# Performance work log

Measured on AMD Instinct MI355X. Metric: run time of the kernel, lower is better.

The kernel has to match this reference:

```python
import jax, jax.numpy as jnp
import numpy as np
import math

M_MICRO = 8    # n_micro
CELLS = 1024   # cells per micro engine (n_cells // n_micro)
DIM = 512      # hidden_dim (complex state dim)
IN_DIM = 512   # input_dim == hidden_dim so torch's F.interpolate branch is skipped


def _build_neighbors(n):
    """Hypercube bit-flip + ring topology, deduped, padded to max degree."""
    n_bits = max(1, int(math.ceil(math.log2(n))))
    lists = []
    for i in range(n):
        s = set()
        for b in range(n_bits):
            j = i ^ (1 << b)
            if 0 <= j < n:
                s.add(j)
        s.add((i + 1) % n)
        s.add((i - 1) % n)
        lists.append(sorted(s))
    K = max(len(l) for l in lists)
    idx = np.zeros((n, K), dtype=np.int32)
    mask = np.zeros((n, K), dtype=np.float32)
    for i, l in enumerate(lists):
        idx[i, : len(l)] = l
        mask[i, : len(l)] = 1.0
    return idx, mask


def _forward(x, step, amp0, phase0, phase_vel, nbr_idx, nbr_mask, macro_h0,
             w_ih, b_ih, w_hh, b_hh, wq, bq, wk, bk, wv, bv, out_w, out_b):
    sig = x.reshape(-1)                    # [DIM]; input_dim == dim -> no interpolation
    t = step * 0.1
    states0 = amp0 * jnp.exp(1j * phase0)  # complex64 [M, n, d]

    def micro_step(st, pv):
        # phase-velocity rotation
        st = st * jnp.exp(1j * (pv * 0.1))
        ang = jnp.angle(st)
        nb_s = st[nbr_idx]                 # [n, K, d] neighbor gather
        nb_a = ang[nbr_idx]
        coupling = jnp.cos(ang[:, None, :] - nb_a)
        interf = jnp.sum(coupling * nb_s * nbr_mask[:, :, None], axis=1) * 0.1
        cnt = jnp.maximum(nbr_mask.sum(axis=1), 1.0)
        new = 0.7 * st + 0.3 * interf / cnt[:, None]
        # category morphism from strongest neighbor (selected on pre-interference states)
        absum = jnp.abs(st).sum(axis=-1)
        score = jnp.where(nbr_mask > 0, absum[nbr_idx], -jnp.inf)
        sel = jnp.argmax(score, axis=1)
        midx = jnp.take_along_axis(nbr_idx, sel[:, None], axis=1)[:, 0]
        src = st[midx]
        morph = jnp.abs(src) * jnp.exp(1j * (jnp.angle(new) - jnp.angle(src)))
        new = new + 0.02 * morph
        # global wave modulation
        i_arr = jnp.arange(new.shape[0], dtype=jnp.float32)
        wave = 0.02 * jnp.sin(t + 2.0 * math.pi * i_arr / new.shape[0])
        new = new * (1.0 + wave)[:, None]
        # signal phase perturbation (per-cell decaying scale)
        sig_norm = sig / (jnp.abs(sig).max() + 1e-8)
        pp = sig_norm * (math.pi * 0.1)
        scale = 0.1 / (1.0 + 0.1 * i_arr)
        newang = jnp.angle(new) + pp[None, :] * scale[:, None]
        # amplitude renormalization
        amp = jnp.abs(new)
        amp = amp / (amp.max(axis=-1, keepdims=True) + 1e-8)
        return amp * jnp.exp(1j * newang)

    states = jax.vmap(micro_step)(states0, phase_vel)  # [M, n, d]
    # micro outputs and coherences are .detach()'ed / .item()'ed in torch
    micro_out = jax.lax.stop_gradient(jnp.abs(states).mean(axis=1))          # [M, d]
    coh = jax.lax.stop_gradient(
        jnp.abs(jnp.exp(1j * jnp.angle(states)).mean(axis=1)).mean(axis=1))  # [M]
    # GRUCell (torch gate order: r, z, n)
    gx = micro_out @ w_ih.T + b_ih
    gh = macro_h0 @ w_hh.T + b_hh
    rx, zx, nx = jnp.split(gx, 3, axis=1)
    rh, zh, nh = jnp.split(gh, 3, axis=1)
    r = jax.nn.sigmoid(rx + rh)
    z = jax.nn.sigmoid(zx + zh)
    ng = jnp.tanh(nx + r * nh)
    h = jax.lax.stop_gradient((1.0 - z) * ng + z * macro_h0)  # detached macro hiddens
    H = h.shape[1]
    Q = h @ wq.T + bq
    K = h @ wk.T + bk
    V = h @ wv.T + bv
    scores = (Q @ K.T) / math.sqrt(H)
    scores = scores * (0.5 + 0.5 * coh[None, :] * coh[:, None])
    attn = jax.nn.softmax(scores, axis=-1)
    attended = (attn @ V).mean(axis=0, keepdims=True)  # [1, H]
    # faction sync/debate (updates hidden state; feeds only tension here)
    n_f = 4
    fs = h.shape[0] // n_f
    hh = h.reshape(n_f, fs, -1)
    hh = 0.85 * hh + 0.15 * hh.mean(axis=1, keepdims=True)
    if step > 5:
        go = hh.mean(axis=1).mean(axis=0)
        dc = max(1, fs // 4)
        hh = hh.at[:, :dc].set(0.85 * hh[:, :dc] + 0.15 * go)
    h2 = hh.reshape(h.shape)
    pred = attended @ out_w.T + out_b  # [1, IN_DIM]
    tension = jnp.var(h2, ddof=1)      # torch .var() is unbiased
    return pred, tension


def setup_inputs():
    key = jax.random.key(0)
    k = jax.random.split(key, 20)
    M, n, d, H, IN = M_MICRO, CELLS, DIM, DIM, IN_DIM
    amp0 = jax.random.uniform(k[0], (M, n, d)) * 0.5 + 0.5
    base = jnp.linspace(0.0, 2.0 * math.pi, d)
    gidx = jnp.arange(M * n, dtype=jnp.float32).reshape(M, n)
    off = 2.0 * math.pi * gidx / (n * 8)
    phase0 = base[None, None, :] + off[..., None] + jax.random.normal(k[1], (M, n, d)) * 0.3
    phase_vel = jax.random.normal(k[2], (M, n, d)) * 0.05
    nbr_idx, nbr_mask = _build_neighbors(n)
    macro_h0 = jax.random.normal(k[3], (M, H)) * 0.1
    s = 1.0 / math.sqrt(H)
    u = lambda kk, shape: jax.random.uniform(kk, shape, minval=-s, maxval=s)
    return {
        "x": jax.random.normal(k[4], (1, IN)),
        "step": 0,
        "amp0": amp0, "phase0": phase0, "phase_vel": phase_vel,
        "nbr_idx": jnp.asarray(nbr_idx), "nbr_mask": jnp.asarray(nbr_mask),
        "macro_h0": macro_h0,
        "w_ih": u(k[5], (3 * H, H)), "b_ih": u(k[6], (3 * H,)),
        "w_hh": u(k[7], (3 * H, H)), "b_hh": u(k[8], (3 * H,)),
        "wq": u(k[9], (H, H)), "bq": u(k[10], (H,)),
        "wk": u(k[11], (H, H)), "bk": u(k[12], (H,)),
        "wv": u(k[13], (H, H)), "bv": u(k[14], (H,)),
        "out_w": u(k[15], (IN, H)), "out_b": u(k[16], (IN,)),
    }


def reference(x, step, amp0, phase0, phase_vel, nbr_idx, nbr_mask, macro_h0,
              w_ih, b_ih, w_hh, b_hh, wq, bq, wk, bk, wv, bv, out_w, out_b):
    return _forward(x, step, amp0, phase0, phase_vel, nbr_idx, nbr_mask, macro_h0,
                    w_ih, b_ih, w_hh, b_hh, wq, bq, wk, bk, wv, bv, out_w, out_b)
```

## Files before the change

kernel.cpp:

```cpp
#include <hip/hip_runtime.h>
#include <hip/hip_fp16.h>
#include <math.h>

#define M_  8
#define N_  1024
#define D_  512
#define H_  512
#define PI_ 3.14159265358979323846f

static const size_t OFF_CHS = 0;
static const size_t OFF_SIG = OFF_CHS + (size_t)M_*N_*D_;
static const size_t OFF_MA  = OFF_SIG + 64;
static const size_t OFF_MZR = OFF_MA  + (size_t)M_*D_;
static const size_t OFF_MZI = OFF_MZR + (size_t)M_*D_;
static const size_t OFF_H   = OFF_MZI + (size_t)M_*D_;
static const size_t OFF_Q   = OFF_H   + (size_t)M_*H_;
static const size_t OFF_K   = OFF_Q   + (size_t)M_*H_;
static const size_t OFF_V   = OFF_K   + (size_t)M_*H_;
static const size_t OFF_ATT = OFF_V   + (size_t)M_*H_;
static const size_t FAST_FLOATS = OFF_ATT + 512;
static const size_t FB_SIG = 0;
static const size_t FB_MA  = FB_SIG + 64;
static const size_t FB_MZR = FB_MA  + (size_t)M_*D_;
static const size_t FB_MZI = FB_MZR + (size_t)M_*D_;
static const size_t FB_H   = FB_MZI + (size_t)M_*D_;
static const size_t FB_Q   = FB_H   + (size_t)M_*H_;
static const size_t FB_K   = FB_Q   + (size_t)M_*H_;
static const size_t FB_V   = FB_K   + (size_t)M_*H_;
static const size_t FB_ATT = FB_V   + (size_t)M_*H_;

struct F8   { float4 a, b; };
struct H2x8 { __half2 h[8]; };

__device__ __forceinline__ void unp8(float* d, const F8& v) {
    d[0]=v.a.x; d[1]=v.a.y; d[2]=v.a.z; d[3]=v.a.w;
    d[4]=v.b.x; d[5]=v.b.y; d[6]=v.b.z; d[7]=v.b.w;
}


__global__ __launch_bounds__(256) void prep_kernel(const float* __restrict__ phase0,
                                                   const float* __restrict__ pv,
                                                   const float* __restrict__ x,
                                                   __half2* __restrict__ chs,
                                                   float* __restrict__ acczero,
                                                   float* __restrict__ sigmax) {
    const int bid = blockIdx.x, tid = threadIdx.x;
    if (bid < 2048) {
        const size_t e = ((size_t)bid * 256 + tid) * 8;
        float ph[8], pw[8];
        unp8(ph, *reinterpret_cast<const F8*>(phase0 + e));
        unp8(pw, *reinterpret_cast<const F8*>(pv + e));
        H2x8 out;
        #pragma unroll
        for (int s = 0; s < 8; ++s) {
            const float th = fmaf(0.1f, pw[s], ph[s]);
            out.h[s] = __floats2half2_rn(__cosf(th), __sinf(th));
        }
        *reinterpret_cast<H2x8*>(chs + e) = out;
        if (bid < 6) {
            F8 z; z.a = make_float4(0.f,0.f,0.f,0.f); z.b = z.a;
            *reinterpret_cast<F8*>(acczero + (size_t)bid * 2048 + (size_t)tid * 8) = z;
        }
    } else if (tid < 64) {
        float v[8];
        unp8(v, *reinterpret_cast<const F8*>(x + (size_t)tid * 8));
        float mx = 0.f;
        #pragma unroll
        for (int s = 0; s < 8; ++s) mx = fmaxf(mx, fabsf(v[s]));
        #pragma unroll
        for (int off = 32; off; off >>= 1) mx = fmaxf(mx, __shfl_down(mx, off));
        if (tid == 0) *sigmax = mx;
    }
}

__global__ __launch_bounds__(512) void micro_kernel(
    const float* __restrict__ amp0, const __half2* __restrict__ chs,
    const float* __restrict__ x, const float* __restrict__ sigmax_p,
    const int* __restrict__ nbr_idx, const float* __restrict__ nbr_mask,
    const int* __restrict__ step_p,
    float* __restrict__ mA, float* __restrict__ mZr, float* __restrict__ mZi, int K)
{
    const int m = blockIdx.x & 7;
    const int g = blockIdx.x >> 3;
    const int wid  = threadIdx.x >> 6;
    const int lane = threadIdx.x & 63;
    const int i = (g << 3) + wid;

    __shared__ float accA[D_], accZr[D_], accZi[D_];
    for (int idx = threadIdx.x; idx < D_; idx += 512) { accA[idx]=0.f; accZr[idx]=0.f; accZi[idx]=0.f; }
    __syncthreads();

    const float t  = 0.1f * (float)(*step_p);
    const float sm = *sigmax_p;

    float pp[8];
    unp8(pp, *reinterpret_cast<const F8*>(x + (size_t)lane * 8));
    #pragma unroll
    for (int s = 0; s < 8; ++s) pp[s] = pp[s] / (sm + 1e-8f) * (PI_ * 0.1f);

    const size_t mrow = (size_t)m * N_;

    int L = 0;
    for (int k = 0; k < K; ++k) L += (nbr_mask[i * K + k] > 0.f) ? 1 : 0;

    float SA[8], SB[8], SC[8];
    #pragma unroll
    for (int s = 0; s < 8; ++s) { SA[s]=0.f; SB[s]=0.f; SC[s]=0.f; }
    float best = -1e30f; int midx = 0;

    for (int k = 0; k < L; ++k) {
        const int nb = nbr_idx[i * K + k];
        const size_t noff = (mrow + nb) * (size_t)D_ + (size_t)lane * 8;
        float aN[8];
        unp8(aN, *reinterpret_cast<const F8*>(amp0 + noff));
        const H2x8 hx = *reinterpret_cast<const H2x8*>(chs + noff);
        #pragma unroll
        for (int s = 0; s < 8; ++s) {
            const float2 cs = __half22float2(hx.h[s]);
            const float ac = aN[s] * cs.x, as_ = aN[s] * cs.y;
            SA[s] = fmaf(ac,  cs.x, SA[s]);
            SB[s] = fmaf(ac,  cs.y, SB[s]);
            SC[s] = fmaf(as_, cs.y, SC[s]);
        }
        float rs = ((aN[0]+aN[1])+(aN[2]+aN[3])) + ((aN[4]+aN[5])+(aN[6]+aN[7]));
        #pragma unroll
        for (int off = 1; off < 64; off <<= 1) rs += __shfl_xor(rs, off);
        const bool sel = rs > best;
        best = sel ? rs : best;
        midx = sel ? nb : midx;
    }
    const float f = 0.03f / fmaxf((float)L, 1.f);

    float nre[8], nim[8];
    {
        const size_t ooff = (mrow + i) * (size_t)D_ + (size_t)lane * 8;
        float aO[8];
        unp8(aO, *reinterpret_cast<const F8*>(amp0 + ooff));
        const H2x8 hx = *reinterpret_cast<const H2x8*>(chs + ooff);
        #pragma unroll
        for (int s = 0; s < 8; ++s) {
            const float2 cs = __half22float2(hx.h[s]);
            nre[s] = 0.7f * aO[s] * cs.x + f * (cs.x * SA[s] + cs.y * SB[s]);
            nim[s] = 0.7f * aO[s] * cs.y + f * (cs.x * SB[s] + cs.y * SC[s]);
        }
    }
    {
        const size_t soff = (mrow + midx) * (size_t)D_ + (size_t)lane * 8;
        float aS[8];
        unp8(aS, *reinterpret_cast<const F8*>(amp0 + soff));
        const H2x8 hx = *reinterpret_cast<const H2x8*>(chs + soff);
        #pragma unroll
        for (int s = 0; s < 8; ++s) {
            const float2 cs = __half22float2(hx.h[s]);
            const float sre = aS[s] * cs.x, sim = aS[s] * cs.y;
            const float inv = __builtin_amdgcn_rcpf(sqrtf(nre[s]*nre[s] + nim[s]*nim[s]));
            const float mre = (nre[s] * sre + nim[s] * sim) * inv;
            const float mim = (nim[s] * sre - nre[s] * sim) * inv;
            nre[s] = fmaf(0.02f, mre, nre[s]);
            nim[s] = fmaf(0.02f, mim, nim[s]);
        }
    }

    const float wf = 1.f + 0.02f * __sinf(t + 2.f * PI_ * (float)i / (float)N_);
    const float scale_i = 0.1f / (1.f + 0.1f * (float)i);

    float ampn[8], rm = 0.f;
    #pragma unroll
    for (int s = 0; s < 8; ++s) {
        nre[s] *= wf; nim[s] *= wf;
        ampn[s] = sqrtf(nre[s]*nre[s] + nim[s]*nim[s]);
        rm = fmaxf(rm, ampn[s]);
    }
    #pragma unroll
    for (int off = 1; off < 64; off <<= 1) rm = fmaxf(rm, __shfl_xor(rm, off));
    const float rinv = __builtin_amdgcn_rcpf(rm + 1e-8f);

    #pragma unroll
    for (int s = 0; s < 8; ++s) {
        const float anorm = ampn[s] * rinv;
        const float iamp  = __builtin_amdgcn_rcpf(ampn[s]);
        const float ure = nre[s] * iamp, uim = nim[s] * iamp;
        const float d  = pp[s] * scale_i;
        const float d2 = d * d;
        const float cd = 1.f - 0.5f * d2;
        const float sd = d * (1.f - 0.16666667f * d2);
        const int p = (s << 6) + lane;
        atomicAdd(&accA[p],  anorm);
        atomicAdd(&accZr[p], ure * cd - uim * sd);
        atomicAdd(&accZi[p], ure * sd + uim * cd);
    }
    __syncthreads();
    const int j = threadIdx.x;
    const int p = ((j & 7) << 6) + (j >> 3);
    atomicAdd(&mA [m * D_ + j], accA[p]);
    atomicAdd(&mZr[m * D_ + j], accZr[p]);
    atomicAdd(&mZi[m * D_ + j], accZi[p]);
}


__global__ __launch_bounds__(256) void zero_sig_kernel(const float* __restrict__ x,
                                                       float* __restrict__ acczero,
                                                       float* __restrict__ sigmax) {
    const int bid = blockIdx.x, tid = threadIdx.x;
    if (bid < 6) {
        F8 z; z.a = make_float4(0.f,0.f,0.f,0.f); z.b = z.a;
        *reinterpret_cast<F8*>(acczero + (size_t)bid * 2048 + (size_t)tid * 8) = z;
    } else if (tid < 64) {
        float v[8];
        unp8(v, *reinterpret_cast<const F8*>(x + (size_t)tid * 8));
        float mx = 0.f;
        #pragma unroll
        for (int s = 0; s < 8; ++s) mx = fmaxf(mx, fabsf(v[s]));
        #pragma unroll
        for (int off = 32; off; off >>= 1) mx = fmaxf(mx, __shfl_down(mx, off));
        if (tid == 0) *sigmax = mx;
    }
}

__global__ __launch_bounds__(512) void micro_fb_kernel(
    const float* __restrict__ amp0, const float* __restrict__ phase0,
    const float* __restrict__ pvel,
    const float* __restrict__ x, const float* __restrict__ sigmax_p,
    const int* __restrict__ nbr_idx, const float* __restrict__ nbr_mask,
    const int* __restrict__ step_p,
    float* __restrict__ mA, float* __restrict__ mZr, float* __restrict__ mZi, int K)
{
    const int m = blockIdx.x & 7;
    const int g = blockIdx.x >> 3;
    const int wid  = threadIdx.x >> 6;
    const int lane = threadIdx.x & 63;
    const int i = (g << 3) + wid;

    __shared__ float accA[D_], accZr[D_], accZi[D_];
    for (int idx = threadIdx.x; idx < D_; idx += 512) { accA[idx]=0.f; accZr[idx]=0.f; accZi[idx]=0.f; }
    __syncthreads();

    const float t  = 0.1f * (float)(*step_p);
    const float sm = *sigmax_p;

    float pp[8];
    unp8(pp, *reinterpret_cast<const F8*>(x + (size_t)lane * 8));
    #pragma unroll
    for (int s = 0; s < 8; ++s) pp[s] = pp[s] / (sm + 1e-8f) * (PI_ * 0.1f);

    const size_t mrow = (size_t)m * N_;

    int L = 0;
    for (int k = 0; k < K; ++k) L += (nbr_mask[i * K + k] > 0.f) ? 1 : 0;

    float SA[8], SB[8], SC[8];
    #pragma unroll
    for (int s = 0; s < 8; ++s) { SA[s]=0.f; SB[s]=0.f; SC[s]=0.f; }
    float best = -1e30f; int midx = 0;

    for (int k = 0; k < L; ++k) {
        const int nb = nbr_idx[i * K + k];
        const size_t noff = (mrow + nb) * (size_t)D_ + (size_t)lane * 8;
        float aN[8], phN[8], pwN[8];
        unp8(aN, *reinterpret_cast<const F8*>(amp0 + noff));
        unp8(phN, *reinterpret_cast<const F8*>(phase0 + noff));
        unp8(pwN, *reinterpret_cast<const F8*>(pvel + noff));
        #pragma unroll
        for (int s = 0; s < 8; ++s) {
            const float th = fmaf(0.1f, pwN[s], phN[s]);
            const float cn = __cosf(th), sn = __sinf(th);
            const float ac = aN[s] * cn, as_ = aN[s] * sn;
            SA[s] = fmaf(ac,  cn, SA[s]);
            SB[s] = fmaf(ac,  sn, SB[s]);
            SC[s] = fmaf(as_, sn, SC[s]);
        }
        float rs = ((aN[0]+aN[1])+(aN[2]+aN[3])) + ((aN[4]+aN[5])+(aN[6]+aN[7]));
        #pragma unroll
        for (int off = 1; off < 64; off <<= 1) rs += __shfl_xor(rs, off);
        const bool sel = rs > best;
        best = sel ? rs : best;
        midx = sel ? nb : midx;
    }
    const float f = 0.03f / fmaxf((float)L, 1.f);

    float nre[8], nim[8];
    {
        const size_t ooff = (mrow + i) * (size_t)D_ + (size_t)lane * 8;
        float aO[8], ph[8], pw[8];
        unp8(aO, *reinterpret_cast<const F8*>(amp0 + ooff));
        unp8(ph, *reinterpret_cast<const F8*>(phase0 + ooff));
        unp8(pw, *reinterpret_cast<const F8*>(pvel + ooff));
        #pragma unroll
        for (int s = 0; s < 8; ++s) {
            const float th = fmaf(0.1f, pw[s], ph[s]);
            const float c = __cosf(th), sn = __sinf(th);
            nre[s] = 0.7f * aO[s] * c  + f * (c * SA[s] + sn * SB[s]);
            nim[s] = 0.7f * aO[s] * sn + f * (c * SB[s] + sn * SC[s]);
        }
    }
    {
        const size_t soff = (mrow + midx) * (size_t)D_ + (size_t)lane * 8;
        float aS[8], ph[8], pw[8];
        unp8(aS, *reinterpret_cast<const F8*>(amp0 + soff));
        unp8(ph, *reinterpret_cast<const F8*>(phase0 + soff));
        unp8(pw, *reinterpret_cast<const F8*>(pvel + soff));
        #pragma unroll
        for (int s = 0; s < 8; ++s) {
            const float th = fmaf(0.1f, pw[s], ph[s]);
            const float c = __cosf(th), sn = __sinf(th);
            const float sre = aS[s] * c, sim = aS[s] * sn;
            const float inv = __builtin_amdgcn_rcpf(sqrtf(nre[s]*nre[s] + nim[s]*nim[s]));
            const float mre = (nre[s] * sre + nim[s] * sim) * inv;
            const float mim = (nim[s] * sre - nre[s] * sim) * inv;
            nre[s] = fmaf(0.02f, mre, nre[s]);
            nim[s] = fmaf(0.02f, mim, nim[s]);
        }
    }

    const float wf = 1.f + 0.02f * __sinf(t + 2.f * PI_ * (float)i / (float)N_);
    const float scale_i = 0.1f / (1.f + 0.1f * (float)i);

    float ampn[8], rm = 0.f;
    #pragma unroll
    for (int s = 0; s < 8; ++s) {
        nre[s] *= wf; nim[s] *= wf;
        ampn[s] = sqrtf(nre[s]*nre[s] + nim[s]*nim[s]);
        rm = fmaxf(rm, ampn[s]);
    }
    #pragma unroll
    for (int off = 1; off < 64; off <<= 1) rm = fmaxf(rm, __shfl_xor(rm, off));
    const float rinv = __builtin_amdgcn_rcpf(rm + 1e-8f);

    #pragma unroll
    for (int s = 0; s < 8; ++s) {
        const float anorm = ampn[s] * rinv;
        const float iamp  = __builtin_amdgcn_rcpf(ampn[s]);
        const float ure = nre[s] * iamp, uim = nim[s] * iamp;
        const float d  = pp[s] * scale_i;
        const float d2 = d * d;
        const float cd = 1.f - 0.5f * d2;
        const float sd = d * (1.f - 0.16666667f * d2);
        const int p = (s << 6) + lane;
        atomicAdd(&accA[p],  anorm);
        atomicAdd(&accZr[p], ure * cd - uim * sd);
        atomicAdd(&accZi[p], ure * sd + uim * cd);
    }
    __syncthreads();
    const int j = threadIdx.x;
    const int p = ((j & 7) << 6) + (j >> 3);
    atomicAdd(&mA [m * D_ + j], accA[p]);
    atomicAdd(&mZr[m * D_ + j], accZr[p]);
    atomicAdd(&mZi[m * D_ + j], accZi[p]);
}


__global__ __launch_bounds__(256) void macro_kernel(
    const float* __restrict__ mA, const float* __restrict__ h0,
    const float* __restrict__ w_ih, const float* __restrict__ b_ih,
    const float* __restrict__ w_hh, const float* __restrict__ b_hh,
    float* __restrict__ h)
{
    __shared__ float vx[M_ * H_], vh[M_ * H_];
    for (int idx = threadIdx.x; idx < M_ * H_; idx += 256) {
        vx[idx] = mA[idx] * (1.f / (float)N_);
        vh[idx] = h0[idx];
    }
    __syncthreads();
    const int wid = threadIdx.x >> 6, lane = threadIdx.x & 63;
    const int d = (blockIdx.x << 2) + wid;
    float wr[6][8];
    #pragma unroll
    for (int rr = 0; rr < 3; ++rr) {
        const size_t row = (size_t)(d + rr * H_) * H_;
        #pragma unroll
        for (int kk = 0; kk < 8; ++kk) {
            wr[rr][kk]     = w_ih[row + kk * 64 + lane];
            wr[rr + 3][kk] = w_hh[row + kk * 64 + lane];
        }
    }
    const float br = b_ih[d], bz = b_ih[d + H_], bn = b_ih[d + 2 * H_];
    const float dr = b_hh[d], dz = b_hh[d + H_], dn = b_hh[d + 2 * H_];
    for (int m = 0; m < M_; ++m) {
        float acc[6] = {0.f, 0.f, 0.f, 0.f, 0.f, 0.f};
        #pragma unroll
        for (int kk = 0; kk < 8; ++kk) {
            const float xm = vx[m * H_ + kk * 64 + lane];
            const float hm = vh[m * H_ + kk * 64 + lane];
            acc[0] = fmaf(wr[0][kk], xm, acc[0]);
            acc[1] = fmaf(wr[1][kk], xm, acc[1]);
            acc[2] = fmaf(wr[2][kk], xm, acc[2]);
            acc[3] = fmaf(wr[3][kk], hm, acc[3]);
            acc[4] = fmaf(wr[4][kk], hm, acc[4]);
            acc[5] = fmaf(wr[5][kk], hm, acc[5]);
        }
        #pragma unroll
        for (int off = 32; off; off >>= 1)
            #pragma unroll
            for (int q = 0; q < 6; ++q) acc[q] += __shfl_down(acc[q], off);
        if (lane == 0) {
            const float r  = 1.f / (1.f + expf(-(acc[0] + br + acc[3] + dr)));
            const float z  = 1.f / (1.f + expf(-(acc[1] + bz + acc[4] + dz)));
            const float ng = tanhf(acc[2] + bn + r * (acc[5] + dn));
            h[m * H_ + d] = (1.f - z) * ng + z * vh[m * H_ + d];
        }
    }
}

__global__ void qkv_kernel(const float* __restrict__ h,
                           const float* __restrict__ wq, const float* __restrict__ bq,
                           const float* __restrict__ wk, const float* __restrict__ bk,
                           const float* __restrict__ wv, const float* __restrict__ bv,
                           float* __restrict__ Q, float* __restrict__ Kk, float* __restrict__ V) {
    __shared__ float hv[M_ * H_];
    for (int idx = threadIdx.x; idx < M_ * H_; idx += blockDim.x) hv[idx] = h[idx];
    __syncthreads();
    const int gr = (blockIdx.x << 2) + (threadIdx.x >> 6);
    const int lane = threadIdx.x & 63;
    const int which = gr / H_, r = gr % H_;
    const float* W = (which == 0) ? wq : ((which == 1) ? wk : wv);
    const float* B = (which == 0) ? bq : ((which == 1) ? bk : bv);
    float* O       = (which == 0) ? Q  : ((which == 1) ? Kk : V);
    float wvv[8];
    #pragma unroll
    for (int kk = 0; kk < 8; ++kk) wvv[kk] = W[(size_t)r * H_ + kk * 64 + lane];
    for (int m = 0; m < M_; ++m) {
        float acc = 0.f;
        #pragma unroll
        for (int kk = 0; kk < 8; ++kk) acc = fmaf(wvv[kk], hv[m * H_ + kk * 64 + lane], acc);
        for (int off = 32; off; off >>= 1) acc += __shfl_down(acc, off);
        if (lane == 0) O[m * H_ + r] = acc + B[r];
    }
}

__global__ void attn_faction_kernel(const float* __restrict__ Q, const float* __restrict__ Kk,
                                    const float* __restrict__ V,
                                    const float* __restrict__ mZr, const float* __restrict__ mZi,
                                    const float* __restrict__ h, const int* __restrict__ step_p,
                                    float* __restrict__ attended, float* __restrict__ out_tension) {
    const int tid = threadIdx.x;
    __shared__ float coh_sm[M_];
    {
        const int w = tid >> 6, lane = tid & 63;
        float s = 0.f;
        #pragma unroll
        for (int q = 0; q < 8; ++q) {
            const int j = lane + (q << 6);
            const float zr = mZr[w * D_ + j], zi = mZi[w * D_ + j];
            s += sqrtf(zr * zr + zi * zi);
        }
        #pragma unroll
        for (int off = 32; off; off >>= 1) s += __shfl_down(s, off);
        if (lane == 0) coh_sm[w] = s * (1.f / ((float)N_ * (float)D_));
    }
    __syncthreads();
    {
        const int j = tid;
        const int step = *step_p;
        float h2[M_];
        #pragma unroll
        for (int ff = 0; ff < 4; ++ff) {
            const float a = h[(2*ff) * H_ + j], b = h[(2*ff+1) * H_ + j];
            const float mn = 0.5f * (a + b);
            h2[2*ff]   = 0.85f * a + 0.15f * mn;
            h2[2*ff+1] = 0.85f * b + 0.15f * mn;
        }
        if (step > 5) {
            float go = 0.f;
            #pragma unroll
            for (int m = 0; m < M_; ++m) go += h2[m];
            go *= (1.f / (float)M_);
            #pragma unroll
            for (int ff = 0; ff < 4; ++ff) h2[2*ff] = 0.85f * h2[2*ff] + 0.15f * go;
        }
        float sum = 0.f, sq = 0.f;
        #pragma unroll
        for (int m = 0; m < M_; ++m) { sum += h2[m]; sq = fmaf(h2[m], h2[m], sq); }
        __shared__ float rs[D_], rq[D_];
        rs[j] = sum; rq[j] = sq;
        __syncthreads();
        for (int s = D_/2; s > 0; s >>= 1) {
            if (j < s) { rs[j] += rs[j + s]; rq[j] += rq[j + s]; }
            __syncthreads();
        }
        if (j == 0) {
            const float Nt = (float)(M_ * H_);
            const float mean = rs[0] / Nt;
            out_tension[0] = (rq[0] - Nt * mean * mean) / (Nt - 1.f);
        }
        __syncthreads();
    }
    __shared__ float sc[M_][M_];
    __shared__ float colw[M_];
    const int a = tid >> 6, lane = tid & 63;
    for (int b = 0; b < M_; ++b) {
        float acc = 0.f;
        #pragma unroll
        for (int kk = 0; kk < 8; ++kk) acc = fmaf(Q[a * H_ + kk * 64 + lane], Kk[b * H_ + kk * 64 + lane], acc);
        for (int off = 32; off; off >>= 1) acc += __shfl_down(acc, off);
        if (lane == 0) sc[a][b] = acc * rsqrtf((float)H_) * (0.5f + 0.5f * coh_sm[a] * coh_sm[b]);
    }
    __syncthreads();
    if (tid < M_) {
        float mx = -1e30f;
        for (int b = 0; b < M_; ++b) mx = fmaxf(mx, sc[tid][b]);
        float e[M_], smm = 0.f;
        for (int b = 0; b < M_; ++b) { e[b] = expf(sc[tid][b] - mx); smm += e[b]; }
        for (int b = 0; b < M_; ++b) sc[tid][b] = e[b] / smm;
    }
    __syncthreads();
    if (tid < M_) {
        float sum = 0.f;
        for (int a2 = 0; a2 < M_; ++a2) sum += sc[a2][tid];
        colw[tid] = sum * (1.f / (float)M_);
    }
    __syncthreads();
    float acc = 0.f;
    #pragma unroll
    for (int b = 0; b < M_; ++b) acc = fmaf(colw[b], V[b * H_ + tid], acc);
    attended[tid] = acc;
}

__global__ void pred_kernel(const float* __restrict__ attended,
                            const float* __restrict__ out_w, const float* __restrict__ out_b,
                            float* __restrict__ pred) {
    __shared__ float av[H_];
    for (int idx = threadIdx.x; idx < H_; idx += blockDim.x) av[idx] = attended[idx];
    __syncthreads();
    const int p = (blockIdx.x << 2) + (threadIdx.x >> 6);
    const int lane = threadIdx.x & 63;
    float acc = 0.f;
    #pragma unroll
    for (int kk = 0; kk < 8; ++kk) acc = fmaf(av[kk * 64 + lane], out_w[(size_t)p * H_ + kk * 64 + lane], acc);
    for (int off = 32; off; off >>= 1) acc += __shfl_down(acc, off);
    if (lane == 0) pred[p] = acc + out_b[p];
}


extern "C" void kernel_launch(void* const* d_in, const int* in_sizes, int n_in,
                              void* d_out, int out_size, void* d_ws, size_t ws_size,
                              hipStream_t stream) {
    const float* x      = (const float*)d_in[0];
    const int*   step   = (const int*)  d_in[1];
    const float* amp0   = (const float*)d_in[2];
    const float* phase0 = (const float*)d_in[3];
    const float* pvel   = (const float*)d_in[4];
    const int*   nbr_i  = (const int*)  d_in[5];
    const float* nbr_m  = (const float*)d_in[6];
    const float* h0     = (const float*)d_in[7];
    const float* w_ih   = (const float*)d_in[8];
    const float* b_ih   = (const float*)d_in[9];
    const float* w_hh   = (const float*)d_in[10];
    const float* b_hh   = (const float*)d_in[11];
    const float* wq     = (const float*)d_in[12];
    const float* bq     = (const float*)d_in[13];
    const float* wk     = (const float*)d_in[14];
    const float* bk     = (const float*)d_in[15];
    const float* wv     = (const float*)d_in[16];
    const float* bv     = (const float*)d_in[17];
    const float* out_w  = (const float*)d_in[18];
    const float* out_b  = (const float*)d_in[19];
    float* out = (float*)d_out;

    const int K = in_sizes[5] / N_;
    float* ws = (float*)d_ws;

    if (ws_size >= FAST_FLOATS * sizeof(float)) {
        __half2* wCHS = (__half2*)(ws + OFF_CHS);
        float* wSIG = ws + OFF_SIG;
        float* wMA  = ws + OFF_MA;
        float* wMZR = ws + OFF_MZR;
        float* wMZI = ws + OFF_MZI;
        float* wH   = ws + OFF_H;
        float* wQ   = ws + OFF_Q;
        float* wK   = ws + OFF_K;
        float* wV   = ws + OFF_V;
        float* wATT = ws + OFF_ATT;

        prep_kernel<<<2049, 256, 0, stream>>>(phase0, pvel, x, wCHS, wMA, wSIG);
        micro_kernel<<<1024, 512, 0, stream>>>(amp0, wCHS, x, wSIG, nbr_i, nbr_m, step,
                                               wMA, wMZR, wMZI, K);
        macro_kernel<<<128, 256, 0, stream>>>(wMA, h0, w_ih, b_ih, w_hh, b_hh, wH);
        qkv_kernel<<<384, 256, 0, stream>>>(wH, wq, bq, wk, bk, wv, bv, wQ, wK, wV);
        attn_faction_kernel<<<1, 512, 0, stream>>>(wQ, wK, wV, wMZR, wMZI, wH, step, wATT, out + 512);
        pred_kernel<<<128, 256, 0, stream>>>(wATT, out_w, out_b, out);
    } else {
        float* wSIG = ws + FB_SIG;
        float* wMA  = ws + FB_MA;
        float* wMZR = ws + FB_MZR;
        float* wMZI = ws + FB_MZI;
        float* wH   = ws + FB_H;
        float* wQ   = ws + FB_Q;
        float* wK   = ws + FB_K;
        float* wV   = ws + FB_V;
        float* wATT = ws + FB_ATT;

        zero_sig_kernel<<<7, 256, 0, stream>>>(x, wMA, wSIG);
        micro_fb_kernel<<<1024, 512, 0, stream>>>(amp0, phase0, pvel, x, wSIG, nbr_i, nbr_m, step,
                                                  wMA, wMZR, wMZI, K);
        macro_kernel<<<128, 256, 0, stream>>>(wMA, h0, w_ih, b_ih, w_hh, b_hh, wH);
        qkv_kernel<<<384, 256, 0, stream>>>(wH, wq, bq, wk, bk, wv, bv, wQ, wK, wV);
        attn_faction_kernel<<<1, 512, 0, stream>>>(wQ, wK, wV, wMZR, wMZI, wH, step, wATT, out + 512);
        pred_kernel<<<128, 256, 0, stream>>>(wATT, out_w, out_b, out);
    }
}
```

Measured before the change: 252.4 us.

## Precompute per-cell amplitude sums in prep and process two cells per wave

The prep kernel now also reads amp0 and writes a per-cell amplitude sum into a new workspace region. The micro kernel uses those sums to pick the strongest neighbor instead of doing a 64-lane shuffle reduction for every neighbor. Each wave now handles two cells, with blocks shrunk to 256 threads. Per-cell contributions are summed in registers before the shared-memory atomics, halving those atomics. In exchange, prep reads amp0 once more, register pressure roughly doubles with two sets of accumulators, and there are fewer waves in flight.

```diff
diff --git a/kernel.cpp b/kernel.cpp
--- a/kernel.cpp
+++ b/kernel.cpp
@@ -13,7 +13,8 @@
 static const size_t OFF_MA  = OFF_SIG + 64;
 static const size_t OFF_MZR = OFF_MA  + (size_t)M_*D_;
 static const size_t OFF_MZI = OFF_MZR + (size_t)M_*D_;
-static const size_t OFF_H   = OFF_MZI + (size_t)M_*D_;
+static const size_t OFF_ABS = OFF_MZI + (size_t)M_*D_;
+static const size_t OFF_H   = OFF_ABS + (size_t)M_*N_;
 static const size_t OFF_Q   = OFF_H   + (size_t)M_*H_;
 static const size_t OFF_K   = OFF_Q   + (size_t)M_*H_;
 static const size_t OFF_V   = OFF_K   + (size_t)M_*H_;
@@ -38,18 +39,21 @@
 }
 
 
-__global__ __launch_bounds__(256) void prep_kernel(const float* __restrict__ phase0,
+__global__ __launch_bounds__(256) void prep_kernel(const float* __restrict__ amp0,
+                                                   const float* __restrict__ phase0,
                                                    const float* __restrict__ pv,
                                                    const float* __restrict__ x,
                                                    __half2* __restrict__ chs,
                                                    float* __restrict__ acczero,
+                                                   float* __restrict__ absum,
                                                    float* __restrict__ sigmax) {
     const int bid = blockIdx.x, tid = threadIdx.x;
     if (bid < 2048) {
         const size_t e = ((size_t)bid * 256 + tid) * 8;
-        float ph[8], pw[8];
+        float ph[8], pw[8], av[8];
         unp8(ph, *reinterpret_cast<const F8*>(phase0 + e));
         unp8(pw, *reinterpret_cast<const F8*>(pv + e));
+        unp8(av, *reinterpret_cast<const F8*>(amp0 + e));
         H2x8 out;
         #pragma unroll
         for (int s = 0; s < 8; ++s) {
@@ -57,6 +61,10 @@
             out.h[s] = __floats2half2_rn(__cosf(th), __sinf(th));
         }
         *reinterpret_cast<H2x8*>(chs + e) = out;
+        float rs = ((av[0]+av[1])+(av[2]+av[3])) + ((av[4]+av[5])+(av[6]+av[7]));
+        #pragma unroll
+        for (int off = 32; off; off >>= 1) rs += __shfl_down(rs, off);
+        if ((tid & 63) == 0) absum[bid * 4 + (tid >> 6)] = rs;
         if (bid < 6) {
             F8 z; z.a = make_float4(0.f,0.f,0.f,0.f); z.b = z.a;
             *reinterpret_cast<F8*>(acczero + (size_t)bid * 2048 + (size_t)tid * 8) = z;
@@ -73,21 +81,26 @@
     }
 }
 
-__global__ __launch_bounds__(512) void micro_kernel(
+__global__ __launch_bounds__(256) void micro_kernel(
     const float* __restrict__ amp0, const __half2* __restrict__ chs,
     const float* __restrict__ x, const float* __restrict__ sigmax_p,
     const int* __restrict__ nbr_idx, const float* __restrict__ nbr_mask,
-    const int* __restrict__ step_p,
+    const int* __restrict__ step_p, const float* __restrict__ absum,
     float* __restrict__ mA, float* __restrict__ mZr, float* __restrict__ mZi, int K)
 {
     const int m = blockIdx.x & 7;
     const int g = blockIdx.x >> 3;
     const int wid  = threadIdx.x >> 6;
     const int lane = threadIdx.x & 63;
-    const int i = (g << 3) + wid;
+    const int i0 = (g << 3) + (wid << 1);
+    const int i1 = i0 + 1;
 
     __shared__ float accA[D_], accZr[D_], accZi[D_];
-    for (int idx = threadIdx.x; idx < D_; idx += 512) { accA[idx]=0.f; accZr[idx]=0.f; accZi[idx]=0.f; }
+    {
+        const int j = threadIdx.x;
+        accA[j] = 0.f; accZr[j] = 0.f; accZi[j] = 0.f;
+        accA[j+256] = 0.f; accZr[j+256] = 0.f; accZi[j+256] = 0.f;
+    }
     __syncthreads();
 
     const float t  = 0.1f * (float)(*step_p);
@@ -99,102 +112,144 @@
     for (int s = 0; s < 8; ++s) pp[s] = pp[s] / (sm + 1e-8f) * (PI_ * 0.1f);
 
     const size_t mrow = (size_t)m * N_;
-
-    int L = 0;
-    for (int k = 0; k < K; ++k) L += (nbr_mask[i * K + k] > 0.f) ? 1 : 0;
-
-    float SA[8], SB[8], SC[8];
-    #pragma unroll
-    for (int s = 0; s < 8; ++s) { SA[s]=0.f; SB[s]=0.f; SC[s]=0.f; }
-    float best = -1e30f; int midx = 0;
-
-    for (int k = 0; k < L; ++k) {
-        const int nb = nbr_idx[i * K + k];
-        const size_t noff = (mrow + nb) * (size_t)D_ + (size_t)lane * 8;
-        float aN[8];
-        unp8(aN, *reinterpret_cast<const F8*>(amp0 + noff));
-        const H2x8 hx = *reinterpret_cast<const H2x8*>(chs + noff);
+    const size_t lo = (size_t)lane * 8;
+
+    int L0 = 0, L1 = 0;
+    for (int k = 0; k < K; ++k) {
+        L0 += (nbr_mask[i0 * K + k] > 0.f) ? 1 : 0;
+        L1 += (nbr_mask[i1 * K + k] > 0.f) ? 1 : 0;
+    }
+    const int Lmax = (L0 > L1) ? L0 : L1;
+
+    float SA0[8], SB0[8], SC0[8], SA1[8], SB1[8], SC1[8];
+    #pragma unroll
+    for (int s = 0; s < 8; ++s) {
+        SA0[s]=0.f; SB0[s]=0.f; SC0[s]=0.f;
+        SA1[s]=0.f; SB1[s]=0.f; SC1[s]=0.f;
+    }
+    float best0 = -1e30f, best1 = -1e30f; int mi0 = 0, mi1 = 0;
+
+    for (int k = 0; k < Lmax; ++k) {
+        const bool v0 = (k < L0), v1 = (k < L1);
+        const int nb0 = v0 ? nbr_idx[i0 * K + k] : 0;
+        const int nb1 = v1 ? nbr_idx[i1 * K + k] : 0;
+        const size_t off0 = (mrow + nb0) * (size_t)D_ + lo;
+        const size_t off1 = (mrow + nb1) * (size_t)D_ + lo;
+        float a0[8], a1[8];
+        unp8(a0, *reinterpret_cast<const F8*>(amp0 + off0));
+        const H2x8 h0 = *reinterpret_cast<const H2x8*>(chs + off0);
+        unp8(a1, *reinterpret_cast<const F8*>(amp0 + off1));
+        const H2x8 h1 = *reinterpret_cast<const H2x8*>(chs + off1);
+        if (v0) {
+            #pragma unroll
+            for (int s = 0; s < 8; ++s) {
+                const float2 cs = __half22float2(h0.h[s]);
+                const float ac = a0[s] * cs.x, as_ = a0[s] * cs.y;
+                SA0[s] = fmaf(ac,  cs.x, SA0[s]);
+                SB0[s] = fmaf(ac,  cs.y, SB0[s]);
+                SC0[s] = fmaf(as_, cs.y, SC0[s]);
+            }
+            const float sc = absum[mrow + nb0];
+            if (sc > best0) { best0 = sc; mi0 = nb0; }
+        }
+        if (v1) {
+            #pragma unroll
+            for (int s = 0; s < 8; ++s) {
+                const float2 cs = __half22float2(h1.h[s]);
+                const float ac = a1[s] * cs.x, as_ = a1[s] * cs.y;
+                SA1[s] = fmaf(ac,  cs.x, SA1[s]);
+                SB1[s] = fmaf(ac,  cs.y, SB1[s]);
+                SC1[s] = fmaf(as_, cs.y, SC1[s]);
+            }
+            const float sc = absum[mrow + nb1];
+            if (sc > best1) { best1 = sc; mi1 = nb1; }
+        }
+    }
+
+    float sA[8], sZr[8], sZi[8];
+    #pragma unroll
+    for (int s = 0; s < 8; ++s) { sA[s]=0.f; sZr[s]=0.f; sZi[s]=0.f; }
+
+    #pragma unroll
+    for (int cc = 0; cc < 2; ++cc) {
+        const int i = cc ? i1 : i0;
+        const int Lc = cc ? L1 : L0;
+        const int mi = cc ? mi1 : mi0;
+        const float f = 0.03f / fmaxf((float)Lc, 1.f);
+        float nre[8], nim[8];
+        {
+            const size_t ooff = (mrow + i) * (size_t)D_ + lo;
+            const size_t soff = (mrow + mi) * (size_t)D_ + lo;
+            float aO[8], aS[8];
+            unp8(aO, *reinterpret_cast<const F8*>(amp0 + ooff));
+            const H2x8 hxo = *reinterpret_cast<const H2x8*>(chs + ooff);
+            unp8(aS, *reinterpret_cast<const F8*>(amp0 + soff));
+            const H2x8 hxs = *reinterpret_cast<const H2x8*>(chs + soff);
+            #pragma unroll
+            for (int s = 0; s < 8; ++s) {
+                const float2 cs = __half22float2(hxo.h[s]);
+                const float* SAp = cc ? SA1 : SA0;
+                const float* SBp = cc ? SB1 : SB0;
+                const float* SCp = cc ? SC1 : SC0;
+                nre[s] = 0.7f * aO[s] * cs.x + f * (cs.x * SAp[s] + cs.y * SBp[s]);
+                nim[s] = 0.7f * aO[s] * cs.y + f * (cs.x * SBp[s] + cs.y * SCp[s]);
+            }
+            #pragma unroll
+            for (int s = 0; s < 8; ++s) {
+                const float2 cs = __half22float2(hxs.h[s]);
+                const float sre = aS[s] * cs.x, sim = aS[s] * cs.y;
+                const float inv = __builtin_amdgcn_rcpf(sqrtf(nre[s]*nre[s] + nim[s]*nim[s]));
+                const float mre = (nre[s] * sre + nim[s] * sim) * inv;
+                const float mim = (nim[s] * sre - nre[s] * sim) * inv;
+                nre[s] = fmaf(0.02f, mre, nre[s]);
+                nim[s] = fmaf(0.02f, mim, nim[s]);
+            }
+        }
+        const float wf = 1.f + 0.02f * __sinf(t + 2.f * PI_ * (float)i / (float)N_);
+        const float scale_i = 0.1f / (1.f + 0.1f * (float)i);
+
+        float ampn[8], rm = 0.f;
         #pragma unroll
         for (int s = 0; s < 8; ++s) {
-            const float2 cs = __half22float2(hx.h[s]);
-            const float ac = aN[s] * cs.x, as_ = aN[s] * cs.y;
-            SA[s] = fmaf(ac,  cs.x, SA[s]);
-            SB[s] = fmaf(ac,  cs.y, SB[s]);
-            SC[s] = fmaf(as_, cs.y, SC[s]);
-        }
-        float rs = ((aN[0]+aN[1])+(aN[2]+aN[3])) + ((aN[4]+aN[5])+(aN[6]+aN[7]));
-        #pragma unroll
-        for (int off = 1; off < 64; off <<= 1) rs += __shfl_xor(rs, off);
-        const bool sel = rs > best;
-        best = sel ? rs : best;
-        midx = sel ? nb : midx;
-    }
-    const float f = 0.03f / fmaxf((float)L, 1.f);
-
-    float nre[8], nim[8];
-    {
-        const size_t ooff = (mrow + i) * (size_t)D_ + (size_t)lane * 8;
-        float aO[8];
-        unp8(aO, *reinterpret_cast<const F8*>(amp0 + ooff));
-        const H2x8 hx = *reinterpret_cast<const H2x8*>(chs + ooff);
+            nre[s] *= wf; nim[s] *= wf;
+            ampn[s] = sqrtf(nre[s]*nre[s] + nim[s]*nim[s]);
+            rm = fmaxf(rm, ampn[s]);
+        }
+        #pragma unroll
+        for (int off = 1; off < 64; off <<= 1) rm = fmaxf(rm, __shfl_xor(rm, off));
+        const float rinv = __builtin_amdgcn_rcpf(rm + 1e-8f);
+
         #pragma unroll
         for (int s = 0; s < 8; ++s) {
-            const float2 cs = __half22float2(hx.h[s]);
-            nre[s] = 0.7f * aO[s] * cs.x + f * (cs.x * SA[s] + cs.y * SB[s]);
-            nim[s] = 0.7f * aO[s] * cs.y + f * (cs.x * SB[s] + cs.y * SC[s]);
-        }
-    }
-    {
-        const size_t soff = (mrow + midx) * (size_t)D_ + (size_t)lane * 8;
-        float aS[8];
-        unp8(aS, *reinterpret_cast<const F8*>(amp0 + soff));
-        const H2x8 hx = *reinterpret_cast<const H2x8*>(chs + soff);
-        #pragma unroll
-        for (int s = 0; s < 8; ++s) {
-            const float2 cs = __half22float2(hx.h[s]);
-            const float sre = aS[s] * cs.x, sim = aS[s] * cs.y;
-            const float inv = __builtin_amdgcn_rcpf(sqrtf(nre[s]*nre[s] + nim[s]*nim[s]));
-            const float mre = (nre[s] * sre + nim[s] * sim) * inv;
-            const float mim = (nim[s] * sre - nre[s] * sim) * inv;
-            nre[s] = fmaf(0.02f, mre, nre[s]);
-            nim[s] = fmaf(0.02f, mim, nim[s]);
-        }
-    }
-
-    const float wf = 1.f + 0.02f * __sinf(t + 2.f * PI_ * (float)i / (float)N_);
-    const float scale_i = 0.1f / (1.f + 0.1f * (float)i);
-
-    float ampn[8], rm = 0.f;
+            const float anorm = ampn[s] * rinv;
+            const float iamp  = __builtin_amdgcn_rcpf(ampn[s]);
+            const float ure = nre[s] * iamp, uim = nim[s] * iamp;
+            const float d  = pp[s] * scale_i;
+            const float d2 = d * d;
+            const float cd = 1.f - 0.5f * d2;
+            const float sd = d * (1.f - 0.16666667f * d2);
+            sA[s]  += anorm;
+            sZr[s] += ure * cd - uim * sd;
+            sZi[s] += ure * sd + uim * cd;
+        }
+    }
+
     #pragma unroll
     for (int s = 0; s < 8; ++s) {
-        nre[s] *= wf; nim[s] *= wf;
-        ampn[s] = sqrtf(nre[s]*nre[s] + nim[s]*nim[s]);
-        rm = fmaxf(rm, ampn[s]);
-    }
-    #pragma unroll
-    for (int off = 1; off < 64; off <<= 1) rm = fmaxf(rm, __shfl_xor(rm, off));
-    const float rinv = __builtin_amdgcn_rcpf(rm + 1e-8f);
-
-    #pragma unroll
-    for (int s = 0; s < 8; ++s) {
-        const float anorm = ampn[s] * rinv;
-        const float iamp  = __builtin_amdgcn_rcpf(ampn[s]);
-        const float ure = nre[s] * iamp, uim = nim[s] * iamp;
-        const float d  = pp[s] * scale_i;
-        const float d2 = d * d;
-        const float cd = 1.f - 0.5f * d2;
-        const float sd = d * (1.f - 0.16666667f * d2);
         const int p = (s << 6) + lane;
-        atomicAdd(&accA[p],  anorm);
-        atomicAdd(&accZr[p], ure * cd - uim * sd);
-        atomicAdd(&accZi[p], ure * sd + uim * cd);
-    }
-    __syncthreads();
-    const int j = threadIdx.x;
-    const int p = ((j & 7) << 6) + (j >> 3);
-    atomicAdd(&mA [m * D_ + j], accA[p]);
-    atomicAdd(&mZr[m * D_ + j], accZr[p]);
-    atomicAdd(&mZi[m * D_ + j], accZi[p]);
+        atomicAdd(&accA[p],  sA[s]);
+        atomicAdd(&accZr[p], sZr[s]);
+        atomicAdd(&accZi[p], sZi[s]);
+    }
+    __syncthreads();
+    #pragma unroll
+    for (int q = 0; q < 2; ++q) {
+        const int j = threadIdx.x + (q << 8);
+        const int p = ((j & 7) << 6) + (j >> 3);
+        atomicAdd(&mA [m * D_ + j], accA[p]);
+        atomicAdd(&mZr[m * D_ + j], accZr[p]);
+        atomicAdd(&mZi[m * D_ + j], accZi[p]);
+    }
 }
 
 
@@ -565,15 +620,16 @@
         float* wMA  = ws + OFF_MA;
         float* wMZR = ws + OFF_MZR;
         float* wMZI = ws + OFF_MZI;
+        float* wABS = ws + OFF_ABS;
         float* wH   = ws + OFF_H;
         float* wQ   = ws + OFF_Q;
         float* wK   = ws + OFF_K;
         float* wV   = ws + OFF_V;
         float* wATT = ws + OFF_ATT;
 
-        prep_kernel<<<2049, 256, 0, stream>>>(phase0, pvel, x, wCHS, wMA, wSIG);
-        micro_kernel<<<1024, 512, 0, stream>>>(amp0, wCHS, x, wSIG, nbr_i, nbr_m, step,
-                                               wMA, wMZR, wMZI, K);
+        prep_kernel<<<2049, 256, 0, stream>>>(amp0, phase0, pvel, x, wCHS, wMA, wABS, wSIG);
+        micro_kernel<<<1024, 256, 0, stream>>>(amp0, wCHS, x, wSIG, nbr_i, nbr_m, step,
+                                               wABS, wMA, wMZR, wMZI, K);
         macro_kernel<<<128, 256, 0, stream>>>(wMA, h0, w_ih, b_ih, w_hh, b_hh, wH);
         qkv_kernel<<<384, 256, 0, stream>>>(wH, wq, bq, wk, bk, wv, bv, wQ, wK, wV);
         attn_faction_kernel<<<1, 512, 0, stream>>>(wQ, wK, wV, wMZR, wMZI, wH, step, wATT, out + 512);
```

After: 217.6 us. 13.8% less time.
